# Performance work log

Hardware: AMD Instinct MI355X
Metric: run time of the kernel (lower is better)

The kernel has to match this reference:

```python
import jax, jax.numpy as jnp
import numpy as np
from jax import lax

CIN, COUT, K_EXP, KSZ = 128, 256, 8, 3
HIDDEN = CIN // 4  # reduction=4
B, H, W = 32, 56, 56
TEMP = 1.0


def setup_inputs() -> dict:
    key = jax.random.key(0)
    ks = jax.random.split(key, 6)
    x = jax.random.normal(ks[0], (B, CIN, H, W), dtype=jnp.float32)
    weight_bank = jax.random.normal(ks[1], (K_EXP, COUT, CIN, KSZ, KSZ), dtype=jnp.float32) * 0.02
    fc1_w = jax.random.normal(ks[2], (HIDDEN, CIN), dtype=jnp.float32) * (1.0 / np.sqrt(CIN))
    fc1_b = jnp.zeros((HIDDEN,), dtype=jnp.float32)
    fc2_w = jax.random.normal(ks[3], (K_EXP, HIDDEN), dtype=jnp.float32) * (1.0 / np.sqrt(HIDDEN))
    fc2_b = jnp.zeros((K_EXP,), dtype=jnp.float32)
    return {"x": x, "weight_bank": weight_bank, "fc1_w": fc1_w, "fc1_b": fc1_b,
            "fc2_w": fc2_w, "fc2_b": fc2_b}


def reference(x, weight_bank, fc1_w, fc1_b, fc2_w, fc2_b):
    b, cin, h, w = x.shape
    # Routing: GAP -> fc1 -> relu -> fc2 -> softmax(/T)
    v = jnp.mean(x, axis=(2, 3))                       # (B, cin)
    hdd = jax.nn.relu(v @ fc1_w.T + fc1_b)             # (B, hidden)
    logits = hdd @ fc2_w.T + fc2_b                     # (B, K)
    a = jax.nn.softmax(logits / TEMP, axis=1)          # (B, K)
    # Per-sample dynamic weights: (B, cout, cin, k, k)
    Wdyn = jnp.einsum('bk,kocij->bocij', a, weight_bank)
    # Batched per-sample conv via grouped convolution:
    # x -> (1, B*cin, H, W), Wdyn -> (B*cout, cin, k, k), groups=B
    xg = x.reshape(1, b * cin, h, w)
    wg = Wdyn.reshape(b * weight_bank.shape[1], cin, KSZ, KSZ)
    y = lax.conv_general_dilated(
        xg, wg,
        window_strides=(1, 1),
        padding=[(1, 1), (1, 1)],
        feature_group_count=b,
        dimension_numbers=('NCHW', 'OIHW', 'NCHW'),
    )
    return y.reshape(b, weight_bank.shape[1], y.shape[2], y.shape[3])
```

## Files before the change

kernel.cpp:

```cpp
#include <hip/hip_runtime.h>


#define CIN    128
#define COUT   256
#define KEXP   8
#define HIDDEN 32
#define B_     32
#define H_     56
#define W_     56
#define HW     3136
#define HP     58
#define WP     58
#define KK     1152

typedef float  v4f  __attribute__((ext_vector_type(4)));
typedef __bf16 v8bf __attribute__((ext_vector_type(8)));

__device__ __forceinline__ unsigned short f2bf(float x) {
  unsigned int u = __float_as_uint(x);
  u += 0x7fff + ((u >> 16) & 1);
  return (unsigned short)(u >> 16);
}

__device__ __forceinline__ void gl_lds16(const void* g, void* lds) {
  __builtin_amdgcn_global_load_lds(
      (__attribute__((address_space(1))) void*)(unsigned long long)(g),
      (__attribute__((address_space(3))) void*)(lds),
      16, 0, 0);
}

__global__ __launch_bounds__(256) void k_xpose(const float* __restrict__ x,
                                               unsigned short* __restrict__ xpt,
                                               float* __restrict__ gpart) {
  const int h = blockIdx.x, b = blockIdx.y, tid = threadIdx.x;
  __shared__ float tf[56 * 129];
  __shared__ float gp[256];
  const float4* xr4 = (const float4*)x + (size_t)b * CIN * 784;

#pragma unroll
  for (int it = 0; it < 7; ++it) {
    int idx = it * 256 + tid;
    int c  = idx / 14;
    int wq = idx - c * 14;
    float4 q = xr4[(size_t)c * 784 + h * 14 + wq];
    int w0 = wq * 4;
    tf[(w0 + 0) * 129 + c] = q.x;
    tf[(w0 + 1) * 129 + c] = q.y;
    tf[(w0 + 2) * 129 + c] = q.z;
    tf[(w0 + 3) * 129 + c] = q.w;
  }
  __syncthreads();

  {
    int c = tid & 127, half = tid >> 7;
    float s = 0.f;
#pragma unroll
    for (int w = half * 28; w < half * 28 + 28; ++w) s += tf[w * 129 + c];
    gp[tid] = s;
  }

#pragma unroll
  for (int it = 0; it < 7; ++it) {
    int idx = it * 256 + tid;
    int w  = idx >> 5;
    int c4 = (idx & 31) << 2;
    ushort4 o;
    o.x = f2bf(tf[w * 129 + c4 + 0]);
    o.y = f2bf(tf[w * 129 + c4 + 1]);
    o.z = f2bf(tf[w * 129 + c4 + 2]);
    o.w = f2bf(tf[w * 129 + c4 + 3]);
    *(ushort4*)(xpt + ((size_t)(b * HP + (h + 1)) * WP + (w + 1)) * CIN + c4) = o;
  }

  if (tid < 128) {
    size_t rb = (size_t)(b * HP + (h + 1)) * WP * CIN;
    xpt[rb + tid] = 0;
    xpt[rb + 57 * CIN + tid] = 0;
  }
  if (h == 0 || h == 55) {
    int hr = (h == 0) ? 0 : 57;
    size_t rb = (size_t)(b * HP + hr) * WP * CIN;
    ushort4 z; z.x = z.y = z.z = z.w = 0;
    for (int i = tid; i < 1856; i += 256)
      *(ushort4*)(xpt + rb + i * 4) = z;
  }

  __syncthreads();
  if (tid < 128)
    gpart[((size_t)h * B_ + b) * CIN + tid] =
        (gp[tid] + gp[tid + 128]) * (1.0f / 3136.0f);
}

__global__ void k_mlp(const float* __restrict__ gpart, const float* __restrict__ fc1w,
                      const float* __restrict__ fc1b, const float* __restrict__ fc2w,
                      const float* __restrict__ fc2b, float* __restrict__ aout) {
  const int b = blockIdx.x, t = threadIdx.x;
  __shared__ float vS[CIN];
  __shared__ float hid[HIDDEN];
  __shared__ float lg[KEXP];
  {
    float s = 0.f;
    for (int h = 0; h < H_; ++h) s += gpart[((size_t)h * B_ + b) * CIN + t];
    vS[t] = s;
  }
  __syncthreads();
  if (t < HIDDEN) {
    float s = fc1b[t];
    const float* wr = fc1w + t * CIN;
    for (int c = 0; c < CIN; ++c) s += vS[c] * wr[c];
    hid[t] = fmaxf(s, 0.f);
  }
  __syncthreads();
  if (t < KEXP) {
    float s = fc2b[t];
    const float* wr = fc2w + t * HIDDEN;
    for (int j = 0; j < HIDDEN; ++j) s += hid[j] * wr[j];
    lg[t] = s;
  }
  __syncthreads();
  if (t == 0) {
    float m = lg[0];
    for (int k = 1; k < KEXP; ++k) m = fmaxf(m, lg[k]);
    float e[KEXP], den = 0.f;
    for (int k = 0; k < KEXP; ++k) { e[k] = expf(lg[k] - m); den += e[k]; }
    float inv = 1.0f / den;
    for (int k = 0; k < KEXP; ++k) aout[b * KEXP + k] = e[k] * inv;
  }
}

__global__ __launch_bounds__(512) void k_wdyn(const float* __restrict__ aout,
                                              const float* __restrict__ bank,
                                              unsigned short* __restrict__ wdyn) {
  const int cout = blockIdx.x, tid = threadIdx.x;
  __shared__ float4 bS4[KEXP * 288];
  __shared__ float aS[B_ * KEXP];

  for (int idx = tid; idx < KEXP * 288; idx += 512) {
    int k = idx / 288, r = idx - k * 288;
    bS4[idx] = ((const float4*)(bank + (size_t)(k * COUT + cout) * KK))[r];
  }
  if (tid < 256) aS[tid] = aout[tid];
  __syncthreads();

  const float* bS = (const float*)bS4;
  const int lane_kk = tid & 63;
  const int sg = tid >> 6;
  float areg[4][KEXP];
#pragma unroll
  for (int bi = 0; bi < 4; ++bi)
#pragma unroll
    for (int k = 0; k < KEXP; ++k) areg[bi][k] = aS[(sg * 4 + bi) * KEXP + k];

  for (int it = 0; it < 18; ++it) {
    int kk  = it * 64 + lane_kk;
    int khw = kk >> 7, cin = kk & 127;
    int e   = cin * 9 + khw;
    float vv[KEXP];
#pragma unroll
    for (int k = 0; k < KEXP; ++k) vv[k] = bS[k * KK + e];
#pragma unroll
    for (int bi = 0; bi < 4; ++bi) {
      float s = 0.f;
#pragma unroll
      for (int k = 0; k < KEXP; ++k) s += areg[bi][k] * vv[k];
      wdyn[(size_t)((sg * 4 + bi) * COUT + cout) * KK + kk] = f2bf(s);
    }
  }
}

#define BARX()   asm volatile("s_barrier" ::: "memory")
#define WAITV4() asm volatile("s_waitcnt vmcnt(4)" ::: "memory")
#define WAITV0() asm volatile("s_waitcnt vmcnt(0)" ::: "memory")

__device__ __forceinline__ void stage4(const unsigned short* src, unsigned short* dbuf,
                                       const int (&off)[4], int disp, int tid) {
#pragma unroll
  for (int g = 0; g < 4; ++g)
    gl_lds16(src + off[g] + disp, dbuf + (g * 256 + tid) * 8);
}

template <int MH>
__device__ __forceinline__ void load_a(const unsigned short* Ab, int abase, int pA, int pB,
                                       v8bf (&af)[2][2]) {
#pragma unroll
  for (int mi = 0; mi < 2; ++mi) {
    int r = abase + (MH * 2 + mi) * 1024;
    af[mi][0] = *(const v8bf*)(Ab + r + pA);
    af[mi][1] = *(const v8bf*)(Ab + r + pB);
  }
}

template <int NH>
__device__ __forceinline__ void load_b(const unsigned short* Bb, int bbase, int pA, int pB,
                                       v8bf (&bv)[2][2]) {
#pragma unroll
  for (int ni = 0; ni < 2; ++ni) {
    int r = bbase + (NH * 2 + ni) * 1024;
    bv[ni][0] = *(const v8bf*)(Bb + r + pA);
    bv[ni][1] = *(const v8bf*)(Bb + r + pB);
  }
}

template <int MH, int NH>
__device__ __forceinline__ void mfma_q(v8bf (&af)[2][2], v8bf (&bv)[2][2],
                                       v4f (&acc)[4][4]) {
  __builtin_amdgcn_s_setprio(1);
#pragma unroll
  for (int mi = 0; mi < 2; ++mi)
#pragma unroll
    for (int ni = 0; ni < 2; ++ni) {
      v4f& a = acc[MH * 2 + mi][NH * 2 + ni];
      a = __builtin_amdgcn_mfma_f32_16x16x32_bf16(af[mi][0], bv[ni][0], a, 0, 0, 0);
      a = __builtin_amdgcn_mfma_f32_16x16x32_bf16(af[mi][1], bv[ni][1], a, 0, 0, 0);
    }
  __builtin_amdgcn_s_setprio(0);
}

__global__ __launch_bounds__(256, 2) void k_conv128(const unsigned short* __restrict__ wdyn,
                                                    const unsigned short* __restrict__ xpt,
                                                    float* __restrict__ out) {
  extern __shared__ unsigned short sh[];
  unsigned short* As = sh;
  unsigned short* Bs = sh + 16384;

  const int id  = blockIdx.x;
  const int xcd = id & 7, idx = id >> 3;
  const int bs  = idx / 50;
  const int r   = idx - bs * 50;
  const int b   = xcd * 4 + bs;
  const int bm  = r / 25;
  const int ch  = r - bm * 25;
  const int p0  = ch << 7;

  const int tid = threadIdx.x;
  const int wv = tid >> 6, l = tid & 63;
  const int q4 = l >> 4, l15 = l & 15;
  const int wr = wv >> 1, wc = wv & 1;

  const unsigned short* wb = wdyn + ((size_t)b * COUT + bm * 128) * KK;
  const unsigned short* xb = xpt + (size_t)b * HP * WP * CIN;

  int aoff[4], boff[4];
#pragma unroll
  for (int g = 0; g < 4; ++g) {
    int gidx = g * 256 + tid;
    int row = gidx >> 3;
    int c = (gidx & 7) ^ (row & 7);
    aoff[g] = row * KK + c * 8;
    int p = p0 + row;
    p = p > 3135 ? 3135 : p;
    int ph = p / 56, pw = p - ph * 56;
    boff[g] = (ph * WP + pw) * CIN + c * 8;
  }

  const int abase = (wr * 64 + l15) * 64;
  const int bbase = (wc * 64 + l15) * 64;
  const int s7 = l15 & 7;
  const int pA = (q4 ^ s7) * 8;
  const int pB = ((q4 + 4) ^ s7) * 8;

  v4f acc[4][4];
#pragma unroll
  for (int m = 0; m < 4; ++m)
#pragma unroll
    for (int n = 0; n < 4; ++n)
#pragma unroll
      for (int rr = 0; rr < 4; ++rr) acc[m][n][rr] = 0.f;

  unsigned short* A0 = As;          unsigned short* B0 = Bs;
  unsigned short* A1 = As + 8192;   unsigned short* B1 = Bs + 8192;

  stage4(wb, A0, aoff, 0, tid);
  stage4(xb, B0, boff, 0, tid);
  WAITV0();
  BARX();

  v8bf afA[2][2], bv0[2][2], bv1[2][2];

  auto tile = [&](const unsigned short* Ab, const unsigned short* Bb,
                  unsigned short* An, unsigned short* Bn,
                  int adS, int bdS, bool doStage) {
    if (doStage) { stage4(wb, An, aoff, adS, tid); WAITV4(); }
    else         { WAITV0(); }
    BARX();
    load_a<0>(Ab, abase, pA, pB, afA);
    load_b<0>(Bb, bbase, pA, pB, bv0);
    mfma_q<0, 0>(afA, bv0, acc);
    load_b<1>(Bb, bbase, pA, pB, bv1);
    if (doStage) stage4(xb, Bn, boff, bdS, tid);
    mfma_q<0, 1>(afA, bv1, acc);
    load_a<1>(Ab, abase, pA, pB, afA);
    mfma_q<1, 1>(afA, bv1, acc);
    mfma_q<1, 0>(afA, bv0, acc);
    BARX();
  };

  int kh = 0, kw = 0;
  for (int i = 0; i < 9; ++i) {
    int kw2 = kw + 1, kh2 = kh;
    if (kw2 == 3) { kw2 = 0; kh2 = kh + 1; }
    const int adO = (2 * i + 1) * 64;
    const int adN = (2 * i + 2) * 64;
    const int bdO = (kh * WP + kw) * CIN + 64;
    const int bdN = (kh2 * WP + kw2) * CIN;

    tile(A0, B0, A1, B1, adO, bdO, true);
    tile(A1, B1, A0, B0, adN, bdN, i != 8);

    kh = kh2; kw = kw2;
  }

#pragma unroll
  for (int mf = 0; mf < 4; ++mf) {
    int cout = bm * 128 + wr * 64 + mf * 16 + 4 * q4;
#pragma unroll
    for (int nf = 0; nf < 4; ++nf) {
      int p = p0 + wc * 64 + nf * 16 + l15;
      if (p < HW) {
        float* op = out + (size_t)(b * COUT + cout) * HW + p;
#pragma unroll
        for (int rr = 0; rr < 4; ++rr) op[(size_t)rr * HW] = acc[mf][nf][rr];
      }
    }
  }
}

extern "C" void kernel_launch(void* const* d_in, const int* in_sizes, int n_in,
                              void* d_out, int out_size, void* d_ws, size_t ws_size,
                              hipStream_t stream) {
  const float* x    = (const float*)d_in[0];
  const float* bank = (const float*)d_in[1];
  const float* fc1w = (const float*)d_in[2];
  const float* fc1b = (const float*)d_in[3];
  const float* fc2w = (const float*)d_in[4];
  const float* fc2b = (const float*)d_in[5];
  float* out = (float*)d_out;

  char* ws = (char*)d_ws;
  float* gpart = (float*)(ws + 0);
  float* aout  = (float*)(ws + (1u << 20));
  unsigned short* wdyn = (unsigned short*)(ws + (2u << 20));
  unsigned short* xpt  = (unsigned short*)(ws + (2u << 20) + 18874368);

  static bool attr_done = false;
  if (!attr_done) {
    (void)hipFuncSetAttribute((const void*)k_conv128,
                              hipFuncAttributeMaxDynamicSharedMemorySize, 65536);
    attr_done = true;
  }

  k_xpose<<<dim3(H_, B_), 256, 0, stream>>>(x, xpt, gpart);
  k_mlp<<<dim3(B_), 128, 0, stream>>>(gpart, fc1w, fc1b, fc2w, fc2b, aout);
  k_wdyn<<<dim3(COUT), 512, 0, stream>>>(aout, bank, wdyn);
  k_conv128<<<dim3(1600), 256, 65536, stream>>>(wdyn, xpt, out);
}
```

Baseline: 223.4 us.

## Switch conv GEMM to 32x32x16 MFMA and stage both operands early

```diff
diff --git a/kernel.cpp b/kernel.cpp
--- a/kernel.cpp
+++ b/kernel.cpp
@@ -14,6 +14,7 @@
 #define KK     1152
 
 typedef float  v4f  __attribute__((ext_vector_type(4)));
+typedef float  v16f __attribute__((ext_vector_type(16)));
 typedef __bf16 v8bf __attribute__((ext_vector_type(8)));
 
 __device__ __forceinline__ unsigned short f2bf(float x) {
@@ -33,7 +34,7 @@
                                                unsigned short* __restrict__ xpt,
                                                float* __restrict__ gpart) {
   const int h = blockIdx.x, b = blockIdx.y, tid = threadIdx.x;
-  __shared__ float tf[56 * 129];
+  __shared__ __align__(16) unsigned short tfb[56 * 132];
   __shared__ float gp[256];
   const float4* xr4 = (const float4*)x + (size_t)b * CIN * 784;
 
@@ -44,10 +45,10 @@
     int wq = idx - c * 14;
     float4 q = xr4[(size_t)c * 784 + h * 14 + wq];
     int w0 = wq * 4;
-    tf[(w0 + 0) * 129 + c] = q.x;
-    tf[(w0 + 1) * 129 + c] = q.y;
-    tf[(w0 + 2) * 129 + c] = q.z;
-    tf[(w0 + 3) * 129 + c] = q.w;
+    tfb[(w0 + 0) * 132 + c] = f2bf(q.x);
+    tfb[(w0 + 1) * 132 + c] = f2bf(q.y);
+    tfb[(w0 + 2) * 132 + c] = f2bf(q.z);
+    tfb[(w0 + 3) * 132 + c] = f2bf(q.w);
   }
   __syncthreads();
 
@@ -55,7 +56,8 @@
     int c = tid & 127, half = tid >> 7;
     float s = 0.f;
 #pragma unroll
-    for (int w = half * 28; w < half * 28 + 28; ++w) s += tf[w * 129 + c];
+    for (int w = half * 28; w < half * 28 + 28; ++w)
+      s += __uint_as_float((unsigned)tfb[w * 132 + c] << 16);
     gp[tid] = s;
   }
 
@@ -64,11 +66,7 @@
     int idx = it * 256 + tid;
     int w  = idx >> 5;
     int c4 = (idx & 31) << 2;
-    ushort4 o;
-    o.x = f2bf(tf[w * 129 + c4 + 0]);
-    o.y = f2bf(tf[w * 129 + c4 + 1]);
-    o.z = f2bf(tf[w * 129 + c4 + 2]);
-    o.w = f2bf(tf[w * 129 + c4 + 3]);
+    ushort4 o = *(const ushort4*)(tfb + w * 132 + c4);
     *(ushort4*)(xpt + ((size_t)(b * HP + (h + 1)) * WP + (w + 1)) * CIN + c4) = o;
   }
 
@@ -169,7 +167,7 @@
 }
 
 #define BARX()   asm volatile("s_barrier" ::: "memory")
-#define WAITV4() asm volatile("s_waitcnt vmcnt(4)" ::: "memory")
+#define WAITV8() asm volatile("s_waitcnt vmcnt(8)" ::: "memory")
 #define WAITV0() asm volatile("s_waitcnt vmcnt(0)" ::: "memory")
 
 __device__ __forceinline__ void stage4(const unsigned short* src, unsigned short* dbuf,
@@ -179,40 +177,18 @@
     gl_lds16(src + off[g] + disp, dbuf + (g * 256 + tid) * 8);
 }
 
-template <int MH>
-__device__ __forceinline__ void load_a(const unsigned short* Ab, int abase, int pA, int pB,
-                                       v8bf (&af)[2][2]) {
-#pragma unroll
-  for (int mi = 0; mi < 2; ++mi) {
-    int r = abase + (MH * 2 + mi) * 1024;
-    af[mi][0] = *(const v8bf*)(Ab + r + pA);
-    af[mi][1] = *(const v8bf*)(Ab + r + pB);
-  }
-}
-
-template <int NH>
-__device__ __forceinline__ void load_b(const unsigned short* Bb, int bbase, int pA, int pB,
-                                       v8bf (&bv)[2][2]) {
-#pragma unroll
-  for (int ni = 0; ni < 2; ++ni) {
-    int r = bbase + (NH * 2 + ni) * 1024;
-    bv[ni][0] = *(const v8bf*)(Bb + r + pA);
-    bv[ni][1] = *(const v8bf*)(Bb + r + pB);
-  }
-}
-
-template <int MH, int NH>
-__device__ __forceinline__ void mfma_q(v8bf (&af)[2][2], v8bf (&bv)[2][2],
-                                       v4f (&acc)[4][4]) {
+__device__ __forceinline__ void load4(const unsigned short* base, const int (&pc)[4],
+                                      v8bf (&f)[4]) {
+#pragma unroll
+  for (int ks = 0; ks < 4; ++ks)
+    f[ks] = *(const v8bf*)(base + pc[ks]);
+}
+
+__device__ __forceinline__ void mfma4(const v8bf (&a)[4], const v8bf (&b)[4], v16f& acc) {
   __builtin_amdgcn_s_setprio(1);
 #pragma unroll
-  for (int mi = 0; mi < 2; ++mi)
-#pragma unroll
-    for (int ni = 0; ni < 2; ++ni) {
-      v4f& a = acc[MH * 2 + mi][NH * 2 + ni];
-      a = __builtin_amdgcn_mfma_f32_16x16x32_bf16(af[mi][0], bv[ni][0], a, 0, 0, 0);
-      a = __builtin_amdgcn_mfma_f32_16x16x32_bf16(af[mi][1], bv[ni][1], a, 0, 0, 0);
-    }
+  for (int ks = 0; ks < 4; ++ks)
+    acc = __builtin_amdgcn_mfma_f32_32x32x16_bf16(a[ks], b[ks], acc, 0, 0, 0);
   __builtin_amdgcn_s_setprio(0);
 }
 
@@ -220,8 +196,10 @@
                                                     const unsigned short* __restrict__ xpt,
                                                     float* __restrict__ out) {
   extern __shared__ unsigned short sh[];
-  unsigned short* As = sh;
-  unsigned short* Bs = sh + 16384;
+  unsigned short* A0 = sh;
+  unsigned short* A1 = sh + 8192;
+  unsigned short* B0 = sh + 16384;
+  unsigned short* B1 = sh + 24576;
 
   const int id  = blockIdx.x;
   const int xcd = id & 7, idx = id >> 3;
@@ -234,7 +212,7 @@
 
   const int tid = threadIdx.x;
   const int wv = tid >> 6, l = tid & 63;
-  const int q4 = l >> 4, l15 = l & 15;
+  const int l31 = l & 31, hi = l >> 5, s7 = l & 7;
   const int wr = wv >> 1, wc = wv & 1;
 
   const unsigned short* wb = wdyn + ((size_t)b * COUT + bm * 128) * KK;
@@ -253,76 +231,70 @@
     boff[g] = (ph * WP + pw) * CIN + c * 8;
   }
 
-  const int abase = (wr * 64 + l15) * 64;
-  const int bbase = (wc * 64 + l15) * 64;
-  const int s7 = l15 & 7;
-  const int pA = (q4 ^ s7) * 8;
-  const int pB = ((q4 + 4) ^ s7) * 8;
-
-  v4f acc[4][4];
-#pragma unroll
-  for (int m = 0; m < 4; ++m)
-#pragma unroll
-    for (int n = 0; n < 4; ++n)
-#pragma unroll
-      for (int rr = 0; rr < 4; ++rr) acc[m][n][rr] = 0.f;
-
-  unsigned short* A0 = As;          unsigned short* B0 = Bs;
-  unsigned short* A1 = As + 8192;   unsigned short* B1 = Bs + 8192;
+  const int abase = (wr * 64 + l31) * 64;
+  const int bbase = (wc * 64 + l31) * 64;
+  int pc[4];
+#pragma unroll
+  for (int ks = 0; ks < 4; ++ks) pc[ks] = ((2 * ks + hi) ^ s7) * 8;
+
+  v16f acc[2][2];
+#pragma unroll
+  for (int mi = 0; mi < 2; ++mi)
+#pragma unroll
+    for (int ni = 0; ni < 2; ++ni)
+#pragma unroll
+      for (int rr = 0; rr < 16; ++rr) acc[mi][ni][rr] = 0.f;
 
   stage4(wb, A0, aoff, 0, tid);
   stage4(xb, B0, boff, 0, tid);
   WAITV0();
   BARX();
 
-  v8bf afA[2][2], bv0[2][2], bv1[2][2];
-
-  auto tile = [&](const unsigned short* Ab, const unsigned short* Bb,
-                  unsigned short* An, unsigned short* Bn,
-                  int adS, int bdS, bool doStage) {
-    if (doStage) { stage4(wb, An, aoff, adS, tid); WAITV4(); }
-    else         { WAITV0(); }
+  v8bf afA[4], bv0[4], bv1[4];
+
+  for (int t = 0; t < 18; ++t) {
+    const unsigned short* Ab = (t & 1) ? A1 : A0;
+    const unsigned short* Bb = (t & 1) ? B1 : B0;
+    unsigned short* An = (t & 1) ? A0 : A1;
+    unsigned short* Bn = (t & 1) ? B0 : B1;
+
+    if (t < 17) {
+      int tn = t + 1;
+      int khw = tn >> 1;
+      int kh = (khw * 11) >> 5;
+      int kw = khw - 3 * kh;
+      stage4(wb, An, aoff, tn * 64, tid);
+      stage4(xb, Bn, boff, (kh * WP + kw) * CIN + ((tn & 1) << 6), tid);
+      WAITV8();
+    } else {
+      WAITV0();
+    }
     BARX();
-    load_a<0>(Ab, abase, pA, pB, afA);
-    load_b<0>(Bb, bbase, pA, pB, bv0);
-    mfma_q<0, 0>(afA, bv0, acc);
-    load_b<1>(Bb, bbase, pA, pB, bv1);
-    if (doStage) stage4(xb, Bn, boff, bdS, tid);
-    mfma_q<0, 1>(afA, bv1, acc);
-    load_a<1>(Ab, abase, pA, pB, afA);
-    mfma_q<1, 1>(afA, bv1, acc);
-    mfma_q<1, 0>(afA, bv0, acc);
+
+    load4(Ab + abase, pc, afA);
+    load4(Bb + bbase, pc, bv0);
+    mfma4(afA, bv0, acc[0][0]);
+    load4(Bb + bbase + 2048, pc, bv1);
+    mfma4(afA, bv1, acc[0][1]);
+    load4(Ab + abase + 2048, pc, afA);
+    mfma4(afA, bv1, acc[1][1]);
+    mfma4(afA, bv0, acc[1][0]);
     BARX();
-  };
-
-  int kh = 0, kw = 0;
-  for (int i = 0; i < 9; ++i) {
-    int kw2 = kw + 1, kh2 = kh;
-    if (kw2 == 3) { kw2 = 0; kh2 = kh + 1; }
-    const int adO = (2 * i + 1) * 64;
-    const int adN = (2 * i + 2) * 64;
-    const int bdO = (kh * WP + kw) * CIN + 64;
-    const int bdN = (kh2 * WP + kw2) * CIN;
-
-    tile(A0, B0, A1, B1, adO, bdO, true);
-    tile(A1, B1, A0, B0, adN, bdN, i != 8);
-
-    kh = kh2; kw = kw2;
-  }
-
-#pragma unroll
-  for (int mf = 0; mf < 4; ++mf) {
-    int cout = bm * 128 + wr * 64 + mf * 16 + 4 * q4;
-#pragma unroll
-    for (int nf = 0; nf < 4; ++nf) {
-      int p = p0 + wc * 64 + nf * 16 + l15;
+  }
+
+#pragma unroll
+  for (int mi = 0; mi < 2; ++mi)
+#pragma unroll
+    for (int ni = 0; ni < 2; ++ni) {
+      int p = p0 + wc * 64 + ni * 32 + l31;
       if (p < HW) {
-        float* op = out + (size_t)(b * COUT + cout) * HW + p;
-#pragma unroll
-        for (int rr = 0; rr < 4; ++rr) op[(size_t)rr * HW] = acc[mf][nf][rr];
+#pragma unroll
+        for (int reg = 0; reg < 16; ++reg) {
+          int cout = bm * 128 + wr * 64 + mi * 32 + (reg & 3) + 8 * (reg >> 2) + 4 * hi;
+          out[(size_t)(b * COUT + cout) * HW + p] = acc[mi][ni][reg];
+        }
       }
     }
-  }
 }
 
 extern "C" void kernel_launch(void* const* d_in, const int* in_sizes, int n_in,
```

After: 241.8 us. 8.2% more time.
